# Kernel tuning notes

Hardware: AMD Instinct MI355X
Metric: run time of the kernel (lower is better)

The kernel has to match this reference:

```python
import jax, jax.numpy as jnp
import numpy as np

N_PAPER, N_AUTHOR = 200000, 100000
D_PAPER, D_AUTHOR = 128, 64
H, OUT = 64, 32
E_CITES, E_WRITES = 4000000, 2000000


def _gcn(x, W, b, src, dst, n):
    # GCNConv with default add_self_loops=True, symmetric normalization
    xl = x @ W
    deg = jnp.zeros((n,), xl.dtype).at[dst].add(1.0) + 1.0  # +1 for self loop
    dis = jax.lax.rsqrt(deg)
    norm = dis[src] * dis[dst]
    out = jax.ops.segment_sum(xl[src] * norm[:, None], dst, num_segments=n)
    out = out + xl * (dis * dis)[:, None]  # self-loop term: norm_ii = 1/deg_i
    return out + b


def _sage(x_src, x_dst, Wl, bl, Wr, src, dst, n_dst):
    # SAGEConv: mean neighbor aggregation -> lin_l, plus root lin_r on dst
    ones = jnp.ones(src.shape, x_src.dtype)
    cnt = jnp.maximum(jax.ops.segment_sum(ones, dst, num_segments=n_dst), 1.0)
    mean = jax.ops.segment_sum(x_src[src], dst, num_segments=n_dst) / cnt[:, None]
    return mean @ Wl + bl + x_dst @ Wr


def _gat(x_src, x_dst, Ws, Wd, a_s, a_d, b, src, dst, n_dst):
    # GATConv heads=1, bipartite, add_self_loops=False, leaky_relu slope 0.2
    xs = x_src @ Ws  # [Ns, H]
    xd = x_dst @ Wd  # [Nd, H]
    a_src = xs @ a_s  # [Ns]
    a_dst = xd @ a_d  # [Nd]
    e = a_src[src] + a_dst[dst]
    e = jnp.where(e > 0, e, 0.2 * e)
    m = jax.ops.segment_max(e, dst, num_segments=n_dst)
    m = jnp.where(jnp.isfinite(m), m, 0.0)  # nodes with no in-edges
    ex = jnp.exp(e - m[dst])
    denom = jax.ops.segment_sum(ex, dst, num_segments=n_dst)
    alpha = ex / denom[dst]
    out = jax.ops.segment_sum(alpha[:, None] * xs[src], dst, num_segments=n_dst)
    return out + b


def _forward(x_paper, x_author, params, cites_src, cites_dst, writes_src, writes_dst):
    for (gW, gb, sWl, sbl, sWr, aWs, aWd, aas, aad, ab) in params:
        p_gcn = _gcn(x_paper, gW, gb, cites_src, cites_dst, N_PAPER)
        p_sage = _sage(x_author, x_paper, sWl, sbl, sWr, writes_src, writes_dst, N_PAPER)
        # rev_writes: paper -> author, i.e. src=writes_dst (paper), dst=writes_src (author)
        a_gat = _gat(x_paper, x_author, aWs, aWd, aas, aad, ab, writes_dst, writes_src, N_AUTHOR)
        x_paper = jax.nn.relu(p_gcn + p_sage)  # HeteroConv aggr='sum'
        x_author = jax.nn.relu(a_gat)
    return x_paper, x_author


def setup_inputs() -> dict:
    key = jax.random.key(0)
    ks = jax.random.split(key, 40)
    rn = lambda i, shp, s=0.1: jax.random.normal(ks[i], shp, jnp.float32) * s
    inp = {}
    inp['x_paper'] = rn(0, (N_PAPER, D_PAPER), 1.0)
    inp['x_author'] = rn(1, (N_AUTHOR, D_AUTHOR), 1.0)
    dims = [(D_PAPER, D_AUTHOR), (H, H)]
    i = 2
    for l, (dp, da) in enumerate(dims):
        inp[f'gcn_W{l}'] = rn(i, (dp, H)); i += 1
        inp[f'gcn_b{l}'] = jnp.zeros((H,), jnp.float32)
        inp[f'sage_Wl{l}'] = rn(i, (da, H)); i += 1
        inp[f'sage_bl{l}'] = jnp.zeros((H,), jnp.float32)
        inp[f'sage_Wr{l}'] = rn(i, (dp, H)); i += 1
        inp[f'gat_Ws{l}'] = rn(i, (dp, H)); i += 1
        inp[f'gat_Wd{l}'] = rn(i, (da, H)); i += 1
        inp[f'gat_as{l}'] = rn(i, (H,)); i += 1
        inp[f'gat_ad{l}'] = rn(i, (H,)); i += 1
        inp[f'gat_b{l}'] = jnp.zeros((H,), jnp.float32)
    inp['lin_W'] = rn(i, (H, OUT)); i += 1
    inp['lin_b'] = jnp.zeros((OUT,), jnp.float32)
    inp['cites_src'] = jax.random.randint(ks[30], (E_CITES,), 0, N_PAPER)
    inp['cites_dst'] = jax.random.randint(ks[31], (E_CITES,), 0, N_PAPER)
    inp['writes_src'] = jax.random.randint(ks[32], (E_WRITES,), 0, N_AUTHOR)
    inp['writes_dst'] = jax.random.randint(ks[33], (E_WRITES,), 0, N_PAPER)
    return inp


def reference(x_paper, x_author,
              gcn_W0, gcn_b0, sage_Wl0, sage_bl0, sage_Wr0,
              gat_Ws0, gat_Wd0, gat_as0, gat_ad0, gat_b0,
              gcn_W1, gcn_b1, sage_Wl1, sage_bl1, sage_Wr1,
              gat_Ws1, gat_Wd1, gat_as1, gat_ad1, gat_b1,
              lin_W, lin_b,
              cites_src, cites_dst, writes_src, writes_dst):
    params = [
        (gcn_W0, gcn_b0, sage_Wl0, sage_bl0, sage_Wr0, gat_Ws0, gat_Wd0, gat_as0, gat_ad0, gat_b0),
        (gcn_W1, gcn_b1, sage_Wl1, sage_bl1, sage_Wr1, gat_Ws1, gat_Wd1, gat_as1, gat_ad1, gat_b1),
    ]
    _, x_author_out = _forward(x_paper, x_author, params, cites_src, cites_dst, writes_src, writes_dst)
    return x_author_out @ lin_W + lin_b
```

## Files before the change

kernel.cpp:

```cpp
#include <hip/hip_runtime.h>
#include <hip/hip_bf16.h>

#define NP 200000
#define NA 100000
#define DP 128
#define HD 64
#define EC 4000000
#define EW 2000000
#define NSCAN (2 * NP + NA)
#define NBUCK 8
#define CAPC 64
#define CAPW 48
#define CAPA 64

typedef __hip_bfloat16 bf16;
typedef __attribute__((ext_vector_type(8))) short short8;
typedef __attribute__((ext_vector_type(4))) float f32x4;

__device__ __forceinline__ float bf2f(bf16 h) { return __bfloat162float(h); }

__device__ __forceinline__ short8 pack8(float4 a, float4 b) {
    union {
        short8 s;
        unsigned u[4];
    } r;
    __hip_bfloat162 h;
    h = __float22bfloat162_rn(float2{a.x, a.y});
    r.u[0] = *reinterpret_cast<unsigned*>(&h);
    h = __float22bfloat162_rn(float2{a.z, a.w});
    r.u[1] = *reinterpret_cast<unsigned*>(&h);
    h = __float22bfloat162_rn(float2{b.x, b.y});
    r.u[2] = *reinterpret_cast<unsigned*>(&h);
    h = __float22bfloat162_rn(float2{b.z, b.w});
    r.u[3] = *reinterpret_cast<unsigned*>(&h);
    return r.s;
}


__global__ __launch_bounds__(256) void fill_pass_kernel(const int* __restrict__ cs,
                                                        const int* __restrict__ cd,
                                                        const int* __restrict__ ws,
                                                        const int* __restrict__ wd,
                                                        int* __restrict__ CUR,
                                                        int* __restrict__ colC,
                                                        int* __restrict__ colWd,
                                                        int* __restrict__ colWa, int bucket) {
    long i = (long)blockIdx.x * 256 + threadIdx.x;
    if (i < EC) {
        int d = __builtin_nontemporal_load(&cd[i]);
        if ((int)(((long)d * NBUCK) / NP) != bucket) return;
        int s = __builtin_nontemporal_load(&cs[i]);
        int pos = atomicAdd(&CUR[d * 4], 1);
        if (pos < CAPC) colC[(size_t)d * CAPC + pos] = s;
    } else if (i < (long)EC + EW) {
        long e = i - EC;
        int d = __builtin_nontemporal_load(&wd[e]);
        if ((int)(((long)d * NBUCK) / NP) != bucket) return;
        int s = __builtin_nontemporal_load(&ws[e]);
        int pos = atomicAdd(&CUR[(NP + d) * 4], 1);
        if (pos < CAPW) colWd[(size_t)d * CAPW + pos] = s;
    } else if (i < (long)EC + 2L * EW) {
        long e = i - EC - EW;
        int a = __builtin_nontemporal_load(&ws[e]);
        if ((int)(((long)a * NBUCK) / NA) != bucket) return;
        int d = __builtin_nontemporal_load(&wd[e]);
        int pos = atomicAdd(&CUR[(2 * NP + a) * 4], 1);
        if (pos < CAPA) colWa[(size_t)a * CAPA + pos] = d;
    }
}

__global__ __launch_bounds__(256) void finalize_kernel(const int* __restrict__ CUR,
                                                       float* __restrict__ dis,
                                                       float* __restrict__ invc) {
    int i = blockIdx.x * 256 + threadIdx.x;
    if (i >= NP) return;
    dis[i] = rsqrtf((float)CUR[i * 4] + 1.0f);
    invc[i] = 1.0f / fmaxf((float)CUR[(NP + i) * 4], 1.0f);
}


__global__ __launch_bounds__(256) void conv_author_kernel(const float* __restrict__ XA,
                                                          const float* __restrict__ wvec,
                                                          bf16* __restrict__ XAbf,
                                                          float* __restrict__ adst) {
    __shared__ float vs[64];
    if (threadIdx.x < 64) vs[threadIdx.x] = wvec[threadIdx.x];
    __syncthreads();
    int r = blockIdx.x * 4 + (threadIdx.x >> 6);
    int lane = threadIdx.x & 63;
    float x = XA[(size_t)r * 64 + lane];
    XAbf[(size_t)r * 64 + lane] = __float2bfloat16(x);
    float p = x * vs[lane];
#pragma unroll
    for (int o = 32; o > 0; o >>= 1) p += __shfl_xor(p, o, 64);
    if (lane == 0) adst[r] = p;
}


__global__ void wprep_kernel(const float* __restrict__ Wg, const float* __restrict__ Wl,
                             const float* __restrict__ Wr, const float* __restrict__ Ws0,
                             const float* __restrict__ Ws1, short* __restrict__ WF) {
    int bid = blockIdx.x;
    int lane = threadIdx.x;
    int q = lane & 15, g = lane >> 4;
    int m, r;
    size_t dst;
    if (bid < 16) {
        m = 0; r = bid; dst = 0;
    } else if (bid < 40) {
        m = 1; r = bid - 16; dst = 8192;
    } else if (bid < 56) {
        m = 2; r = bid - 40; dst = 20480;
    } else {
        m = 3; r = bid - 56; dst = 28672;
    }
    int ks = r >> 2, n = r & 3;
    int col = n * 16 + q;
    float v[8];
#pragma unroll
    for (int j = 0; j < 8; j++) {
        int kr = ks * 32 + g * 8 + j;
        float x;
        if (m == 0) x = Wg[(size_t)kr * 64 + col];
        else if (m == 1) x = (kr < 64) ? Wl[(size_t)kr * 64 + col] : Wr[(size_t)(kr - 64) * 64 + col];
        else if (m == 2) x = Ws0[(size_t)kr * 64 + col];
        else x = Ws1[(size_t)kr * 64 + col];
        v[j] = x;
    }
    short8 s = pack8(float4{v[0], v[1], v[2], v[3]}, float4{v[4], v[5], v[6], v[7]});
    *reinterpret_cast<short8*>(WF + dst + ((size_t)r * 64 + lane) * 8) = s;
}


template <int K, bool ABF16, bool ADOT>
__global__ __launch_bounds__(256) void mfma_gemm_kernel(const void* __restrict__ Xv,
                                                        const short* __restrict__ Wf,
                                                        bf16* __restrict__ outb,
                                                        const float* __restrict__ avec,
                                                        float* __restrict__ adot) {
    int tid = threadIdx.x;
    int lane = tid & 63, q = lane & 15, g = lane >> 4;
    int rw = blockIdx.x * 64 + (tid >> 6) * 16;
    int arow = rw + q;
    f32x4 acc[4];
#pragma unroll
    for (int n = 0; n < 4; n++) acc[n] = f32x4{0.f, 0.f, 0.f, 0.f};
#pragma unroll
    for (int ks = 0; ks < K / 32; ks++) {
        short8 af;
        if constexpr (ABF16) {
            af = *reinterpret_cast<const short8*>((const bf16*)Xv + (size_t)arow * K + ks * 32 +
                                                  g * 8);
        } else {
            const float* xr = (const float*)Xv + (size_t)arow * K + ks * 32 + g * 8;
            float4 a0 = *reinterpret_cast<const float4*>(xr);
            float4 a1 = *reinterpret_cast<const float4*>(xr + 4);
            af = pack8(a0, a1);
        }
#pragma unroll
        for (int n = 0; n < 4; n++) {
            short8 bfr = *reinterpret_cast<const short8*>(Wf + ((size_t)(ks * 4 + n) * 64 + lane) * 8);
            acc[n] = __builtin_amdgcn_mfma_f32_16x16x32_bf16(af, bfr, acc[n], 0, 0, 0);
        }
    }
    float av[4];
    if constexpr (ADOT) {
#pragma unroll
        for (int n = 0; n < 4; n++) av[n] = avec[n * 16 + q];
    }
#pragma unroll
    for (int j = 0; j < 4; j++) {
        int R = rw + g * 4 + j;
#pragma unroll
        for (int n = 0; n < 4; n++) {
            outb[(size_t)R * 64 + n * 16 + q] = __float2bfloat16(acc[n][j]);
        }
        if constexpr (ADOT) {
            float t = acc[0][j] * av[0] + acc[1][j] * av[1] + acc[2][j] * av[2] + acc[3][j] * av[3];
            t += __shfl_xor(t, 1, 64);
            t += __shfl_xor(t, 2, 64);
            t += __shfl_xor(t, 4, 64);
            t += __shfl_xor(t, 8, 64);
            if (q == 0) adot[R] = t;
        }
    }
}


__global__ __launch_bounds__(256) void mfma_sage_kernel(const bf16* B3bf,
                                                        const float* __restrict__ XP,
                                                        const float* __restrict__ B2,
                                                        const float* __restrict__ bl,
                                                        const short* __restrict__ Wf, bf16* P1) {
    int tid = threadIdx.x;
    int lane = tid & 63, q = lane & 15, g = lane >> 4;
    int rw = blockIdx.x * 64 + (tid >> 6) * 16;
    int arow = rw + q;
    f32x4 acc[4];
#pragma unroll
    for (int n = 0; n < 4; n++) acc[n] = f32x4{0.f, 0.f, 0.f, 0.f};
#pragma unroll
    for (int ks = 0; ks < 6; ks++) {
        short8 af;
        if (ks < 2) {
            af = *reinterpret_cast<const short8*>(B3bf + (size_t)arow * 64 + ks * 32 + g * 8);
        } else {
            const float* xr = XP + (size_t)arow * DP + (ks - 2) * 32 + g * 8;
            float4 a0 = *reinterpret_cast<const float4*>(xr);
            float4 a1 = *reinterpret_cast<const float4*>(xr + 4);
            af = pack8(a0, a1);
        }
#pragma unroll
        for (int n = 0; n < 4; n++) {
            short8 bfr = *reinterpret_cast<const short8*>(Wf + ((size_t)(ks * 4 + n) * 64 + lane) * 8);
            acc[n] = __builtin_amdgcn_mfma_f32_16x16x32_bf16(af, bfr, acc[n], 0, 0, 0);
        }
    }
    float blv[4];
#pragma unroll
    for (int n = 0; n < 4; n++) blv[n] = bl[n * 16 + q];
#pragma unroll
    for (int j = 0; j < 4; j++) {
        int R = rw + g * 4 + j;
#pragma unroll
        for (int n = 0; n < 4; n++) {
            int col = n * 16 + q;
            float v = acc[n][j] + B2[(size_t)R * 64 + col] + blv[n];
            P1[(size_t)R * 64 + col] = __float2bfloat16(fmaxf(v, 0.f));
        }
    }
}


__global__ __launch_bounds__(256) void gcn_gather_kernel(const bf16* __restrict__ B1,
                                                         const int* __restrict__ CUR,
                                                         const int* __restrict__ colC,
                                                         const float* __restrict__ dis,
                                                         const float* __restrict__ gb,
                                                         float* __restrict__ B2) {
    int node = __builtin_amdgcn_readfirstlane(blockIdx.x * 4 + (threadIdx.x >> 6));
    int lane = threadIdx.x & 63;
    int deg = min(CUR[node * 4], CAPC);
    const int* col = colC + (size_t)node * CAPC;
    float dd = dis[node];
    float self = bf2f(B1[(size_t)node * 64 + lane]);
    float acc = 0.f;
    int e = 0;
    for (; e + 8 <= deg; e += 8) {
        int s[8];
#pragma unroll
        for (int j = 0; j < 8; j++) s[j] = col[e + j];
        float n[8], v[8];
#pragma unroll
        for (int j = 0; j < 8; j++) n[j] = dis[s[j]];
#pragma unroll
        for (int j = 0; j < 8; j++) v[j] = bf2f(B1[(size_t)s[j] * 64 + lane]);
#pragma unroll
        for (int j = 0; j < 8; j++) acc += n[j] * v[j];
    }
    for (; e + 4 <= deg; e += 4) {
        int s0 = col[e], s1 = col[e + 1], s2 = col[e + 2], s3 = col[e + 3];
        float n0 = dis[s0], n1 = dis[s1], n2 = dis[s2], n3 = dis[s3];
        float v0 = bf2f(B1[(size_t)s0 * 64 + lane]);
        float v1 = bf2f(B1[(size_t)s1 * 64 + lane]);
        float v2 = bf2f(B1[(size_t)s2 * 64 + lane]);
        float v3 = bf2f(B1[(size_t)s3 * 64 + lane]);
        acc += n0 * v0 + n1 * v1;
        acc += n2 * v2 + n3 * v3;
    }
    for (; e < deg; e++) {
        int s = col[e];
        acc += dis[s] * bf2f(B1[(size_t)s * 64 + lane]);
    }
    B2[(size_t)node * 64 + lane] = acc * dd + self * dd * dd + gb[lane];
}


__global__ __launch_bounds__(256) void sage_gather_kernel(const bf16* __restrict__ XA,
                                                          const int* __restrict__ CUR,
                                                          const int* __restrict__ colWd,
                                                          const float* __restrict__ invc,
                                                          bf16* __restrict__ B3bf) {
    int node = __builtin_amdgcn_readfirstlane(blockIdx.x * 4 + (threadIdx.x >> 6));
    int lane = threadIdx.x & 63;
    int deg = min(CUR[(NP + node) * 4], CAPW);
    const int* col = colWd + (size_t)node * CAPW;
    float acc = 0.f;
    int e = 0;
    for (; e + 8 <= deg; e += 8) {
        int s[8];
#pragma unroll
        for (int j = 0; j < 8; j++) s[j] = col[e + j];
        float v[8];
#pragma unroll
        for (int j = 0; j < 8; j++) v[j] = bf2f(XA[(size_t)s[j] * 64 + lane]);
#pragma unroll
        for (int j = 0; j < 8; j++) acc += v[j];
    }
    for (; e < deg; e++) acc += bf2f(XA[(size_t)col[e] * 64 + lane]);
    B3bf[(size_t)node * 64 + lane] = __float2bfloat16(acc * invc[node]);
}


__global__ void matvec64_kernel(const float* __restrict__ Wd, const float* __restrict__ ad,
                                float* __restrict__ wvec) {
    int k = threadIdx.x;
    if (k >= 64) return;
    float s = 0.f;
    for (int c = 0; c < 64; c++) s += Wd[k * 64 + c] * ad[c];
    wvec[k] = s;
}

__device__ __forceinline__ float lrelu(float v) { return v > 0.f ? v : 0.2f * v; }


__global__ __launch_bounds__(256) void gat_l0_kernel(const bf16* __restrict__ XS,
                                                     const int* __restrict__ CUR,
                                                     const int* __restrict__ colA,
                                                     const float* __restrict__ asrc,
                                                     float* __restrict__ adst,
                                                     const float* __restrict__ ab,
                                                     const float* __restrict__ wvec1,
                                                     float* __restrict__ outA) {
    int a = __builtin_amdgcn_readfirstlane(blockIdx.x * 4 + (threadIdx.x >> 6));
    int lane = threadIdx.x & 63;
    int deg = min(CUR[(2 * NP + a) * 4], CAPA);
    const int* col = colA + (size_t)a * CAPA;
    float ada = adst[a];
    float acc = 0.f, den = 0.f;
    int e = 0;
    for (; e + 8 <= deg; e += 8) {
        int p[8];
#pragma unroll
        for (int j = 0; j < 8; j++) p[j] = col[e + j];
        float x[8], v[8];
#pragma unroll
        for (int j = 0; j < 8; j++) x[j] = __expf(lrelu(asrc[p[j]] + ada));
#pragma unroll
        for (int j = 0; j < 8; j++) v[j] = bf2f(XS[(size_t)p[j] * 64 + lane]);
#pragma unroll
        for (int j = 0; j < 8; j++) {
            den += x[j];
            acc += x[j] * v[j];
        }
    }
    for (; e < deg; e++) {
        int p = col[e];
        float x = __expf(lrelu(asrc[p] + ada));
        den += x;
        acc += x * bf2f(XS[(size_t)p * 64 + lane]);
    }
    float inv = den > 0.f ? 1.f / den : 0.f;
    float val = fmaxf(acc * inv + ab[lane], 0.f);
    outA[(size_t)a * 64 + lane] = val;
    float pr = val * wvec1[lane];
#pragma unroll
    for (int o = 32; o > 0; o >>= 1) pr += __shfl_xor(pr, o, 64);
    if (lane == 0) adst[a] = pr;
}


__global__ __launch_bounds__(256) void gat_final_kernel(const bf16* __restrict__ XS,
                                                        const int* __restrict__ CUR,
                                                        const int* __restrict__ colA,
                                                        const float* __restrict__ asrc,
                                                        const float* __restrict__ adst,
                                                        const float* __restrict__ ab,
                                                        const float* __restrict__ linW,
                                                        const float* __restrict__ linb,
                                                        float* __restrict__ out) {
    __shared__ float Ws[64 * 32];
    __shared__ float vbuf[4][64];
    __shared__ float lbs[32];
    int tid = threadIdx.x;
    for (int i = tid; i < 64 * 32; i += 256) Ws[i] = linW[i];
    if (tid < 32) lbs[tid] = linb[tid];
    __syncthreads();
    int wid = tid >> 6;
    int a = __builtin_amdgcn_readfirstlane(blockIdx.x * 4 + wid);
    int lane = tid & 63;
    int deg = min(CUR[(2 * NP + a) * 4], CAPA);
    const int* col = colA + (size_t)a * CAPA;
    float ada = adst[a];
    float acc = 0.f, den = 0.f;
    int e = 0;
    for (; e + 8 <= deg; e += 8) {
        int p[8];
#pragma unroll
        for (int j = 0; j < 8; j++) p[j] = col[e + j];
        float x[8], v[8];
#pragma unroll
        for (int j = 0; j < 8; j++) x[j] = __expf(lrelu(asrc[p[j]] + ada));
#pragma unroll
        for (int j = 0; j < 8; j++) v[j] = bf2f(XS[(size_t)p[j] * 64 + lane]);
#pragma unroll
        for (int j = 0; j < 8; j++) {
            den += x[j];
            acc += x[j] * v[j];
        }
    }
    for (; e < deg; e++) {
        int p = col[e];
        float x = __expf(lrelu(asrc[p] + ada));
        den += x;
        acc += x * bf2f(XS[(size_t)p * 64 + lane]);
    }
    float inv = den > 0.f ? 1.f / den : 0.f;
    vbuf[wid][lane] = fmaxf(acc * inv + ab[lane], 0.f);
    __syncthreads();
    if (tid < 128) {
        int w = tid >> 5, c = tid & 31;
        int node = blockIdx.x * 4 + w;
        float s = lbs[c];
#pragma unroll
        for (int k = 0; k < 64; k++) s += vbuf[w][k] * Ws[k * 32 + c];
        out[(size_t)node * 32 + c] = s;
    }
}


static inline int cdivi(long a, long b) { return (int)((a + b - 1) / b); }

extern "C" void kernel_launch(void* const* d_in, const int* in_sizes, int n_in, void* d_out,
                              int out_size, void* d_ws, size_t ws_size, hipStream_t stream) {
    const float* x_paper = (const float*)d_in[0];
    const float* x_author = (const float*)d_in[1];
    const float* gcn_W0 = (const float*)d_in[2];
    const float* gcn_b0 = (const float*)d_in[3];
    const float* sage_Wl0 = (const float*)d_in[4];
    const float* sage_bl0 = (const float*)d_in[5];
    const float* sage_Wr0 = (const float*)d_in[6];
    const float* gat_Ws0 = (const float*)d_in[7];
    const float* gat_Wd0 = (const float*)d_in[8];
    const float* gat_as0 = (const float*)d_in[9];
    const float* gat_ad0 = (const float*)d_in[10];
    const float* gat_b0 = (const float*)d_in[11];
    const float* gat_Ws1 = (const float*)d_in[17];
    const float* gat_Wd1 = (const float*)d_in[18];
    const float* gat_as1 = (const float*)d_in[19];
    const float* gat_ad1 = (const float*)d_in[20];
    const float* gat_b1 = (const float*)d_in[21];
    const float* lin_W = (const float*)d_in[22];
    const float* lin_b = (const float*)d_in[23];
    const int* cites_src = (const int*)d_in[24];
    const int* cites_dst = (const int*)d_in[25];
    const int* writes_src = (const int*)d_in[26];
    const int* writes_dst = (const int*)d_in[27];

    float* out = (float*)d_out;

    char* base = (char*)d_ws;
    bf16* BF = (bf16*)base;
    base += (size_t)NP * 64 * 2;
    float* B2 = (float*)base;
    base += (size_t)NP * 64 * 4;
    int* colC = (int*)base;
    bf16* B3bf = (bf16*)base;
    base += (size_t)NP * CAPC * 4;
    int* colWd = (int*)base;
    float* B5 = (float*)base;
    base += (size_t)NP * CAPW * 4;
    int* colWa = (int*)base;
    base += (size_t)NA * CAPA * 4;
    bf16* XAbf = (bf16*)base;
    base += (size_t)NA * 64 * 2;
    int* CUR = (int*)base;
    base += (size_t)NSCAN * 4 * 4;
    float* dis_p = (float*)base;
    float* invc = dis_p + NP;
    float* asrc = invc + NP;
    float* adst = asrc + NP;
    float* wvec0 = adst + NA;
    float* wvec1 = wvec0 + 64;
    short* WF = (short*)(wvec1 + 64);

    dim3 blk(256);
    const long ETOT = (long)EC + 2L * EW;

    hipMemsetAsync(CUR, 0, (size_t)NSCAN * 4 * 4, stream);
    matvec64_kernel<<<1, 64, 0, stream>>>(gat_Wd0, gat_ad0, wvec0);
    matvec64_kernel<<<1, 64, 0, stream>>>(gat_Wd1, gat_ad1, wvec1);
    wprep_kernel<<<64, 64, 0, stream>>>(gcn_W0, sage_Wl0, sage_Wr0, gat_Ws0, gat_Ws1, WF);

    for (int b = 0; b < NBUCK; b++) {
        fill_pass_kernel<<<cdivi(ETOT, 256), blk, 0, stream>>>(cites_src, cites_dst, writes_src,
                                                               writes_dst, CUR, colC, colWd,
                                                               colWa, b);
    }
    finalize_kernel<<<cdivi(NP, 256), blk, 0, stream>>>(CUR, dis_p, invc);

    conv_author_kernel<<<NA / 4, blk, 0, stream>>>(x_author, wvec0, XAbf, adst);

    mfma_gemm_kernel<DP, false, false><<<NP / 64, blk, 0, stream>>>(x_paper, WF, BF, nullptr,
                                                                    nullptr);
    gcn_gather_kernel<<<NP / 4, blk, 0, stream>>>(BF, CUR, colC, dis_p, gcn_b0, B2);

    sage_gather_kernel<<<NP / 4, blk, 0, stream>>>(XAbf, CUR, colWd, invc, B3bf);
    mfma_sage_kernel<<<NP / 64, blk, 0, stream>>>(B3bf, x_paper, B2, sage_bl0, WF + 8192, B3bf);

    mfma_gemm_kernel<DP, false, true><<<NP / 64, blk, 0, stream>>>(x_paper, WF + 20480, BF,
                                                                   gat_as0, asrc);
    gat_l0_kernel<<<NA / 4, blk, 0, stream>>>(BF, CUR, colWa, asrc, adst, gat_b0, wvec1, B5);

    mfma_gemm_kernel<HD, true, true><<<NP / 64, blk, 0, stream>>>(B3bf, WF + 28672, BF, gat_as1,
                                                                  asrc);
    gat_final_kernel<<<NA / 4, blk, 0, stream>>>(BF, CUR, colWa, asrc, adst, gat_b1, lin_W, lin_b,
                                                 out);
}
```

Baseline: 944.4 us.

## Overlap CSR fill passes with GCN GEMM and author conversion; half-wave gathers

Each of the eight bucketed fill passes now also runs a slice of the first GCN GEMM and of the author bf16 conversion inside one hybrid kernel, so latency-bound atomic scatter work overlaps with compute. The writes-edge pass reads each edge once and fills both the paper-side and author-side adjacency lists, which cuts index reads. The gather kernels now split the 64 lanes into two halves that each handle alternate neighbours with bf16 pair loads, then combine the halves with a cross-lane shuffle. The risks are branch divergence inside the hybrid kernel, higher register pressure from launch_bounds(256,8), and a changed floating-point summation order.

```diff
diff --git a/kernel.cpp b/kernel.cpp
--- a/kernel.cpp
+++ b/kernel.cpp
@@ -13,11 +13,26 @@
 #define CAPW 48
 #define CAPA 64
 
+#define FILLB ((EC + EW + 255) / 256)
+#define NRB (NP / 64)
+#define GB ((NRB + NBUCK - 1) / NBUCK)
+#define CONVB (NA / 4 / NBUCK)
+
 typedef __hip_bfloat16 bf16;
 typedef __attribute__((ext_vector_type(8))) short short8;
 typedef __attribute__((ext_vector_type(4))) float f32x4;
 
 __device__ __forceinline__ float bf2f(bf16 h) { return __bfloat162float(h); }
+
+__device__ __forceinline__ float2 bfpair(const bf16* p) {
+    __hip_bfloat162 h = *reinterpret_cast<const __hip_bfloat162*>(p);
+    return __bfloat1622float2(h);
+}
+
+__device__ __forceinline__ void bfstore2(bf16* p, float x, float y) {
+    __hip_bfloat162 h = __float22bfloat162_rn(float2{x, y});
+    *reinterpret_cast<unsigned*>(p) = *reinterpret_cast<unsigned*>(&h);
+}
 
 __device__ __forceinline__ short8 pack8(float4 a, float4 b) {
     union {
@@ -37,35 +52,102 @@
 }
 
 
-__global__ __launch_bounds__(256) void fill_pass_kernel(const int* __restrict__ cs,
-                                                        const int* __restrict__ cd,
-                                                        const int* __restrict__ ws,
-                                                        const int* __restrict__ wd,
-                                                        int* __restrict__ CUR,
-                                                        int* __restrict__ colC,
-                                                        int* __restrict__ colWd,
-                                                        int* __restrict__ colWa, int bucket) {
-    long i = (long)blockIdx.x * 256 + threadIdx.x;
-    if (i < EC) {
-        int d = __builtin_nontemporal_load(&cd[i]);
-        if ((int)(((long)d * NBUCK) / NP) != bucket) return;
-        int s = __builtin_nontemporal_load(&cs[i]);
-        int pos = atomicAdd(&CUR[d * 4], 1);
-        if (pos < CAPC) colC[(size_t)d * CAPC + pos] = s;
-    } else if (i < (long)EC + EW) {
-        long e = i - EC;
-        int d = __builtin_nontemporal_load(&wd[e]);
-        if ((int)(((long)d * NBUCK) / NP) != bucket) return;
-        int s = __builtin_nontemporal_load(&ws[e]);
-        int pos = atomicAdd(&CUR[(NP + d) * 4], 1);
-        if (pos < CAPW) colWd[(size_t)d * CAPW + pos] = s;
-    } else if (i < (long)EC + 2L * EW) {
-        long e = i - EC - EW;
-        int a = __builtin_nontemporal_load(&ws[e]);
-        if ((int)(((long)a * NBUCK) / NA) != bucket) return;
-        int d = __builtin_nontemporal_load(&wd[e]);
-        int pos = atomicAdd(&CUR[(2 * NP + a) * 4], 1);
-        if (pos < CAPA) colWa[(size_t)a * CAPA + pos] = d;
+template <int K, bool ABF16, bool ADOT>
+__device__ __forceinline__ void mfma_body(const void* __restrict__ Xv,
+                                          const short* __restrict__ Wf, bf16* __restrict__ outb,
+                                          const float* __restrict__ avec,
+                                          float* __restrict__ adot, int rowblock, int tid) {
+    int lane = tid & 63, q = lane & 15, g = lane >> 4;
+    int rw = rowblock * 64 + (tid >> 6) * 16;
+    int arow = rw + q;
+    f32x4 acc[4];
+#pragma unroll
+    for (int n = 0; n < 4; n++) acc[n] = f32x4{0.f, 0.f, 0.f, 0.f};
+#pragma unroll
+    for (int ks = 0; ks < K / 32; ks++) {
+        short8 af;
+        if constexpr (ABF16) {
+            af = *reinterpret_cast<const short8*>((const bf16*)Xv + (size_t)arow * K + ks * 32 +
+                                                  g * 8);
+        } else {
+            const float* xr = (const float*)Xv + (size_t)arow * K + ks * 32 + g * 8;
+            float4 a0 = *reinterpret_cast<const float4*>(xr);
+            float4 a1 = *reinterpret_cast<const float4*>(xr + 4);
+            af = pack8(a0, a1);
+        }
+#pragma unroll
+        for (int n = 0; n < 4; n++) {
+            short8 bfr =
+                *reinterpret_cast<const short8*>(Wf + ((size_t)(ks * 4 + n) * 64 + lane) * 8);
+            acc[n] = __builtin_amdgcn_mfma_f32_16x16x32_bf16(af, bfr, acc[n], 0, 0, 0);
+        }
+    }
+    float av[4];
+    if constexpr (ADOT) {
+#pragma unroll
+        for (int n = 0; n < 4; n++) av[n] = avec[n * 16 + q];
+    }
+#pragma unroll
+    for (int j = 0; j < 4; j++) {
+        int R = rw + g * 4 + j;
+#pragma unroll
+        for (int n = 0; n < 4; n++) {
+            outb[(size_t)R * 64 + n * 16 + q] = __float2bfloat16(acc[n][j]);
+        }
+        if constexpr (ADOT) {
+            float t = acc[0][j] * av[0] + acc[1][j] * av[1] + acc[2][j] * av[2] + acc[3][j] * av[3];
+            t += __shfl_xor(t, 1, 64);
+            t += __shfl_xor(t, 2, 64);
+            t += __shfl_xor(t, 4, 64);
+            t += __shfl_xor(t, 8, 64);
+            if (q == 0) adot[R] = t;
+        }
+    }
+}
+
+
+__global__ __launch_bounds__(256, 8) void hybrid_kernel(
+    const int* __restrict__ cs, const int* __restrict__ cd, const int* __restrict__ ws,
+    const int* __restrict__ wd, int* __restrict__ CUR, int* __restrict__ colC,
+    int* __restrict__ colWd, int* __restrict__ colWa, int bucket, const float* __restrict__ XP,
+    const short* __restrict__ WFg, bf16* __restrict__ BF, const float* __restrict__ XA,
+    const float* __restrict__ wvec0, bf16* __restrict__ XAbf, float* __restrict__ adst) {
+    int bid = blockIdx.x;
+    int tid = threadIdx.x;
+    if (bid < FILLB) {
+        long i = (long)bid * 256 + tid;
+        if (i < EC) {
+            int d = __builtin_nontemporal_load(&cd[i]);
+            if ((int)(((long)d * NBUCK) / NP) != bucket) return;
+            int s = __builtin_nontemporal_load(&cs[i]);
+            int pos = atomicAdd(&CUR[d * 4], 1);
+            if (pos < CAPC) colC[(size_t)d * CAPC + pos] = s;
+        } else if (i < (long)EC + EW) {
+            long e = i - EC;
+            int d = __builtin_nontemporal_load(&wd[e]);
+            int a = __builtin_nontemporal_load(&ws[e]);
+            if ((int)(((long)d * NBUCK) / NP) == bucket) {
+                int pos = atomicAdd(&CUR[(NP + d) * 4], 1);
+                if (pos < CAPW) colWd[(size_t)d * CAPW + pos] = a;
+            }
+            if ((int)(((long)a * NBUCK) / NA) == bucket) {
+                int pos = atomicAdd(&CUR[(2 * NP + a) * 4], 1);
+                if (pos < CAPA) colWa[(size_t)a * CAPA + pos] = d;
+            }
+        }
+    } else if (bid < FILLB + GB) {
+        int rb = bucket * GB + (bid - FILLB);
+        if (rb >= NRB) return;
+        mfma_body<DP, false, false>(XP, WFg, BF, nullptr, nullptr, rb, tid);
+    } else {
+        int a = (bucket * CONVB + (bid - FILLB - GB)) * 4 + (tid >> 6);
+        int lane = tid & 63;
+        float x = XA[(size_t)a * 64 + lane];
+        XAbf[(size_t)a * 64 + lane] = __float2bfloat16(x);
+        float p = x * wvec0[lane];
+#pragma unroll
+        for (int o = 32; o > 0; o >>= 1) p += __shfl_xor(p, o, 64);
+        if (lane == 0) adst[a] = p;
     }
 }
 
@@ -76,24 +158,6 @@
     if (i >= NP) return;
     dis[i] = rsqrtf((float)CUR[i * 4] + 1.0f);
     invc[i] = 1.0f / fmaxf((float)CUR[(NP + i) * 4], 1.0f);
-}
-
-
-__global__ __launch_bounds__(256) void conv_author_kernel(const float* __restrict__ XA,
-                                                          const float* __restrict__ wvec,
-                                                          bf16* __restrict__ XAbf,
-                                                          float* __restrict__ adst) {
-    __shared__ float vs[64];
-    if (threadIdx.x < 64) vs[threadIdx.x] = wvec[threadIdx.x];
-    __syncthreads();
-    int r = blockIdx.x * 4 + (threadIdx.x >> 6);
-    int lane = threadIdx.x & 63;
-    float x = XA[(size_t)r * 64 + lane];
-    XAbf[(size_t)r * 64 + lane] = __float2bfloat16(x);
-    float p = x * vs[lane];
-#pragma unroll
-    for (int o = 32; o > 0; o >>= 1) p += __shfl_xor(p, o, 64);
-    if (lane == 0) adst[r] = p;
 }
 
 
@@ -138,52 +202,7 @@
                                                         bf16* __restrict__ outb,
                                                         const float* __restrict__ avec,
                                                         float* __restrict__ adot) {
-    int tid = threadIdx.x;
-    int lane = tid & 63, q = lane & 15, g = lane >> 4;
-    int rw = blockIdx.x * 64 + (tid >> 6) * 16;
-    int arow = rw + q;
-    f32x4 acc[4];
-#pragma unroll
-    for (int n = 0; n < 4; n++) acc[n] = f32x4{0.f, 0.f, 0.f, 0.f};
-#pragma unroll
-    for (int ks = 0; ks < K / 32; ks++) {
-        short8 af;
-        if constexpr (ABF16) {
-            af = *reinterpret_cast<const short8*>((const bf16*)Xv + (size_t)arow * K + ks * 32 +
-                                                  g * 8);
-        } else {
-            const float* xr = (const float*)Xv + (size_t)arow * K + ks * 32 + g * 8;
-            float4 a0 = *reinterpret_cast<const float4*>(xr);
-            float4 a1 = *reinterpret_cast<const float4*>(xr + 4);
-            af = pack8(a0, a1);
-        }
-#pragma unroll
-        for (int n = 0; n < 4; n++) {
-            short8 bfr = *reinterpret_cast<const short8*>(Wf + ((size_t)(ks * 4 + n) * 64 + lane) * 8);
-            acc[n] = __builtin_amdgcn_mfma_f32_16x16x32_bf16(af, bfr, acc[n], 0, 0, 0);
-        }
-    }
-    float av[4];
-    if constexpr (ADOT) {
-#pragma unroll
-        for (int n = 0; n < 4; n++) av[n] = avec[n * 16 + q];
-    }
-#pragma unroll
-    for (int j = 0; j < 4; j++) {
-        int R = rw + g * 4 + j;
-#pragma unroll
-        for (int n = 0; n < 4; n++) {
-            outb[(size_t)R * 64 + n * 16 + q] = __float2bfloat16(acc[n][j]);
-        }
-        if constexpr (ADOT) {
-            float t = acc[0][j] * av[0] + acc[1][j] * av[1] + acc[2][j] * av[2] + acc[3][j] * av[3];
-            t += __shfl_xor(t, 1, 64);
-            t += __shfl_xor(t, 2, 64);
-            t += __shfl_xor(t, 4, 64);
-            t += __shfl_xor(t, 8, 64);
-            if (q == 0) adot[R] = t;
-        }
-    }
+    mfma_body<K, ABF16, ADOT>(Xv, Wf, outb, avec, adot, blockIdx.x, threadIdx.x);
 }
 
 
@@ -212,7 +231,8 @@
         }
 #pragma unroll
         for (int n = 0; n < 4; n++) {
-            short8 bfr = *reinterpret_cast<const short8*>(Wf + ((size_t)(ks * 4 + n) * 64 + lane) * 8);
+            short8 bfr =
+                *reinterpret_cast<const short8*>(Wf + ((size_t)(ks * 4 + n) * 64 + lane) * 8);
             acc[n] = __builtin_amdgcn_mfma_f32_16x16x32_bf16(af, bfr, acc[n], 0, 0, 0);
         }
     }
@@ -240,39 +260,46 @@
                                                          float* __restrict__ B2) {
     int node = __builtin_amdgcn_readfirstlane(blockIdx.x * 4 + (threadIdx.x >> 6));
     int lane = threadIdx.x & 63;
+    int half = lane >> 5, c = lane & 31;
     int deg = min(CUR[node * 4], CAPC);
     const int* col = colC + (size_t)node * CAPC;
     float dd = dis[node];
-    float self = bf2f(B1[(size_t)node * 64 + lane]);
-    float acc = 0.f;
+    float2 acc = {0.f, 0.f};
     int e = 0;
-    for (; e + 8 <= deg; e += 8) {
+    for (; e + 16 <= deg; e += 16) {
         int s[8];
 #pragma unroll
-        for (int j = 0; j < 8; j++) s[j] = col[e + j];
-        float n[8], v[8];
+        for (int j = 0; j < 8; j++) s[j] = col[e + 2 * j + half];
+        float n[8];
 #pragma unroll
         for (int j = 0; j < 8; j++) n[j] = dis[s[j]];
-#pragma unroll
-        for (int j = 0; j < 8; j++) v[j] = bf2f(B1[(size_t)s[j] * 64 + lane]);
-#pragma unroll
-        for (int j = 0; j < 8; j++) acc += n[j] * v[j];
-    }
-    for (; e + 4 <= deg; e += 4) {
-        int s0 = col[e], s1 = col[e + 1], s2 = col[e + 2], s3 = col[e + 3];
-        float n0 = dis[s0], n1 = dis[s1], n2 = dis[s2], n3 = dis[s3];
-        float v0 = bf2f(B1[(size_t)s0 * 64 + lane]);
-        float v1 = bf2f(B1[(size_t)s1 * 64 + lane]);
-        float v2 = bf2f(B1[(size_t)s2 * 64 + lane]);
-        float v3 = bf2f(B1[(size_t)s3 * 64 + lane]);
-        acc += n0 * v0 + n1 * v1;
-        acc += n2 * v2 + n3 * v3;
-    }
-    for (; e < deg; e++) {
-        int s = col[e];
-        acc += dis[s] * bf2f(B1[(size_t)s * 64 + lane]);
-    }
-    B2[(size_t)node * 64 + lane] = acc * dd + self * dd * dd + gb[lane];
+        float2 v[8];
+#pragma unroll
+        for (int j = 0; j < 8; j++) v[j] = bfpair(B1 + (size_t)s[j] * 64 + 2 * c);
+#pragma unroll
+        for (int j = 0; j < 8; j++) {
+            acc.x += n[j] * v[j].x;
+            acc.y += n[j] * v[j].y;
+        }
+    }
+    for (; e < deg; e += 2) {
+        int idx = e + half;
+        bool act = idx < deg;
+        int s = col[act ? idx : e];
+        float n = act ? dis[s] : 0.f;
+        float2 v = bfpair(B1 + (size_t)s * 64 + 2 * c);
+        acc.x += n * v.x;
+        acc.y += n * v.y;
+    }
+    acc.x += __shfl_xor(acc.x, 32, 64);
+    acc.y += __shfl_xor(acc.y, 32, 64);
+    if (half == 0) {
+        float2 self = bfpair(B1 + (size_t)node * 64 + 2 * c);
+        float2 o;
+        o.x = acc.x * dd + self.x * dd * dd + gb[2 * c];
+        o.y = acc.y * dd + self.y * dd * dd + gb[2 * c + 1];
+        *reinterpret_cast<float2*>(B2 + (size_t)node * 64 + 2 * c) = o;
+    }
 }
 
 
@@ -283,22 +310,39 @@
                                                           bf16* __restrict__ B3bf) {
     int node = __builtin_amdgcn_readfirstlane(blockIdx.x * 4 + (threadIdx.x >> 6));
     int lane = threadIdx.x & 63;
+    int half = lane >> 5, c = lane & 31;
     int deg = min(CUR[(NP + node) * 4], CAPW);
     const int* col = colWd + (size_t)node * CAPW;
-    float acc = 0.f;
+    float2 acc = {0.f, 0.f};
     int e = 0;
-    for (; e + 8 <= deg; e += 8) {
+    for (; e + 16 <= deg; e += 16) {
         int s[8];
 #pragma unroll
-        for (int j = 0; j < 8; j++) s[j] = col[e + j];
-        float v[8];
-#pragma unroll
-        for (int j = 0; j < 8; j++) v[j] = bf2f(XA[(size_t)s[j] * 64 + lane]);
-#pragma unroll
-        for (int j = 0; j < 8; j++) acc += v[j];
-    }
-    for (; e < deg; e++) acc += bf2f(XA[(size_t)col[e] * 64 + lane]);
-    B3bf[(size_t)node * 64 + lane] = __float2bfloat16(acc * invc[node]);
+        for (int j = 0; j < 8; j++) s[j] = col[e + 2 * j + half];
+        float2 v[8];
+#pragma unroll
+        for (int j = 0; j < 8; j++) v[j] = bfpair(XA + (size_t)s[j] * 64 + 2 * c);
+#pragma unroll
+        for (int j = 0; j < 8; j++) {
+            acc.x += v[j].x;
+            acc.y += v[j].y;
+        }
+    }
+    for (; e < deg; e += 2) {
+        int idx = e + half;
+        bool act = idx < deg;
+        int s = col[act ? idx : e];
+        float2 v = bfpair(XA + (size_t)s * 64 + 2 * c);
+        float n = act ? 1.f : 0.f;
+        acc.x += n * v.x;
+        acc.y += n * v.y;
+    }
+    acc.x += __shfl_xor(acc.x, 32, 64);
+    acc.y += __shfl_xor(acc.y, 32, 64);
+    if (half == 0) {
+        float ic = invc[node];
+        bfstore2(B3bf + (size_t)node * 64 + 2 * c, acc.x * ic, acc.y * ic);
+    }
 }
 
 
@@ -324,39 +368,56 @@
                                                      float* __restrict__ outA) {
     int a = __builtin_amdgcn_readfirstlane(blockIdx.x * 4 + (threadIdx.x >> 6));
     int lane = threadIdx.x & 63;
+    int half = lane >> 5, c = lane & 31;
     int deg = min(CUR[(2 * NP + a) * 4], CAPA);
     const int* col = colA + (size_t)a * CAPA;
     float ada = adst[a];
-    float acc = 0.f, den = 0.f;
+    float2 acc = {0.f, 0.f};
+    float den = 0.f;
     int e = 0;
-    for (; e + 8 <= deg; e += 8) {
-        int p[8];
-#pragma unroll
-        for (int j = 0; j < 8; j++) p[j] = col[e + j];
-        float x[8], v[8];
-#pragma unroll
-        for (int j = 0; j < 8; j++) x[j] = __expf(lrelu(asrc[p[j]] + ada));
-#pragma unroll
-        for (int j = 0; j < 8; j++) v[j] = bf2f(XS[(size_t)p[j] * 64 + lane]);
+    for (; e + 16 <= deg; e += 16) {
+        int s[8];
+#pragma unroll
+        for (int j = 0; j < 8; j++) s[j] = col[e + 2 * j + half];
+        float x[8];
+#pragma unroll
+        for (int j = 0; j < 8; j++) x[j] = __expf(lrelu(asrc[s[j]] + ada));
+        float2 v[8];
+#pragma unroll
+        for (int j = 0; j < 8; j++) v[j] = bfpair(XS + (size_t)s[j] * 64 + 2 * c);
 #pragma unroll
         for (int j = 0; j < 8; j++) {
             den += x[j];
-            acc += x[j] * v[j];
-        }
-    }
-    for (; e < deg; e++) {
-        int p = col[e];
-        float x = __expf(lrelu(asrc[p] + ada));
+            acc.x += x[j] * v[j].x;
+            acc.y += x[j] * v[j].y;
+        }
+    }
+    for (; e < deg; e += 2) {
+        int idx = e + half;
+        bool act = idx < deg;
+        int s = col[act ? idx : e];
+        float x = act ? __expf(lrelu(asrc[s] + ada)) : 0.f;
+        float2 v = bfpair(XS + (size_t)s * 64 + 2 * c);
         den += x;
-        acc += x * bf2f(XS[(size_t)p * 64 + lane]);
-    }
+        acc.x += x * v.x;
+        acc.y += x * v.y;
+    }
+    acc.x += __shfl_xor(acc.x, 32, 64);
+    acc.y += __shfl_xor(acc.y, 32, 64);
+    den += __shfl_xor(den, 32, 64);
     float inv = den > 0.f ? 1.f / den : 0.f;
-    float val = fmaxf(acc * inv + ab[lane], 0.f);
-    outA[(size_t)a * 64 + lane] = val;
-    float pr = val * wvec1[lane];
-#pragma unroll
-    for (int o = 32; o > 0; o >>= 1) pr += __shfl_xor(pr, o, 64);
-    if (lane == 0) adst[a] = pr;
+    float vx = fmaxf(acc.x * inv + ab[2 * c], 0.f);
+    float vy = fmaxf(acc.y * inv + ab[2 * c + 1], 0.f);
+    float pr = vx * wvec1[2 * c] + vy * wvec1[2 * c + 1];
+    pr += __shfl_xor(pr, 1, 64);
+    pr += __shfl_xor(pr, 2, 64);
+    pr += __shfl_xor(pr, 4, 64);
+    pr += __shfl_xor(pr, 8, 64);
+    pr += __shfl_xor(pr, 16, 64);
+    if (half == 0) {
+        *reinterpret_cast<float2*>(outA + (size_t)a * 64 + 2 * c) = float2{vx, vy};
+        if (c == 0) adst[a] = pr;
+    }
 }
 
 
@@ -379,42 +440,56 @@
     int wid = tid >> 6;
     int a = __builtin_amdgcn_readfirstlane(blockIdx.x * 4 + wid);
     int lane = tid & 63;
+    int half = lane >> 5, c = lane & 31;
     int deg = min(CUR[(2 * NP + a) * 4], CAPA);
     const int* col = colA + (size_t)a * CAPA;
     float ada = adst[a];
-    float acc = 0.f, den = 0.f;
+    float2 acc = {0.f, 0.f};
+    float den = 0.f;
     int e = 0;
-    for (; e + 8 <= deg; e += 8) {
-        int p[8];
-#pragma unroll
-        for (int j = 0; j < 8; j++) p[j] = col[e + j];
-        float x[8], v[8];
-#pragma unroll
-        for (int j = 0; j < 8; j++) x[j] = __expf(lrelu(asrc[p[j]] + ada));
-#pragma unroll
-        for (int j = 0; j < 8; j++) v[j] = bf2f(XS[(size_t)p[j] * 64 + lane]);
+    for (; e + 16 <= deg; e += 16) {
+        int s[8];
+#pragma unroll
+        for (int j = 0; j < 8; j++) s[j] = col[e + 2 * j + half];
+        float x[8];
+#pragma unroll
+        for (int j = 0; j < 8; j++) x[j] = __expf(lrelu(asrc[s[j]] + ada));
+        float2 v[8];
+#pragma unroll
+        for (int j = 0; j < 8; j++) v[j] = bfpair(XS + (size_t)s[j] * 64 + 2 * c);
 #pragma unroll
         for (int j = 0; j < 8; j++) {
             den += x[j];
-            acc += x[j] * v[j];
-        }
-    }
-    for (; e < deg; e++) {
-        int p = col[e];
-        float x = __expf(lrelu(asrc[p] + ada));
+            acc.x += x[j] * v[j].x;
+            acc.y += x[j] * v[j].y;
+        }
+    }
+    for (; e < deg; e += 2) {
+        int idx = e + half;
+        bool act = idx < deg;
+        int s = col[act ? idx : e];
+        float x = act ? __expf(lrelu(asrc[s] + ada)) : 0.f;
+        float2 v = bfpair(XS + (size_t)s * 64 + 2 * c);
         den += x;
-        acc += x * bf2f(XS[(size_t)p * 64 + lane]);
-    }
+        acc.x += x * v.x;
+        acc.y += x * v.y;
+    }
+    acc.x += __shfl_xor(acc.x, 32, 64);
+    acc.y += __shfl_xor(acc.y, 32, 64);
+    den += __shfl_xor(den, 32, 64);
     float inv = den > 0.f ? 1.f / den : 0.f;
-    vbuf[wid][lane] = fmaxf(acc * inv + ab[lane], 0.f);
+    if (half == 0) {
+        vbuf[wid][2 * c] = fmaxf(acc.x * inv + ab[2 * c], 0.f);
+        vbuf[wid][2 * c + 1] = fmaxf(acc.y * inv + ab[2 * c + 1], 0.f);
+    }
     __syncthreads();
     if (tid < 128) {
-        int w = tid >> 5, c = tid & 31;
+        int w = tid >> 5, cc = tid & 31;
         int node = blockIdx.x * 4 + w;
-        float s = lbs[c];
-#pragma unroll
-        for (int k = 0; k < 64; k++) s += vbuf[w][k] * Ws[k * 32 + c];
-        out[(size_t)node * 32 + c] = s;
+        float s = lbs[cc];
+#pragma unroll
+        for (int k = 0; k < 64; k++) s += vbuf[w][k] * Ws[k * 32 + cc];
+        out[(size_t)node * 32 + cc] = s;
     }
 }
 
@@ -475,7 +550,6 @@
     short* WF = (short*)(wvec1 + 64);
 
     dim3 blk(256);
-    const long ETOT = (long)EC + 2L * EW;
 
     hipMemsetAsync(CUR, 0, (size_t)NSCAN * 4 * 4, stream);
     matvec64_kernel<<<1, 64, 0, stream>>>(gat_Wd0, gat_ad0, wvec0);
@@ -483,27 +557,23 @@
     wprep_kernel<<<64, 64, 0, stream>>>(gcn_W0, sage_Wl0, sage_Wr0, gat_Ws0, gat_Ws1, WF);
 
     for (int b = 0; b < NBUCK; b++) {
-        fill_pass_kernel<<<cdivi(ETOT, 256), blk, 0, stream>>>(cites_src, cites_dst, writes_src,
-                                                               writes_dst, CUR, colC, colWd,
-                                                               colWa, b);
+        hybrid_kernel<<<FILLB + GB + CONVB, blk, 0, stream>>>(
+            cites_src, cites_dst, writes_src, writes_dst, CUR, colC, colWd, colWa, b, x_paper, WF,
+            BF, x_author, wvec0, XAbf, adst);
     }
     finalize_kernel<<<cdivi(NP, 256), blk, 0, stream>>>(CUR, dis_p, invc);
 
-    conv_author_kernel<<<NA / 4, blk, 0, stream>>>(x_author, wvec0, XAbf, adst);
-
-    mfma_gemm_kernel<DP, false, false><<<NP / 64, blk, 0, stream>>>(x_paper, WF, BF, nullptr,
-                                                                    nullptr);
     gcn_gather_kernel<<<NP / 4, blk, 0, stream>>>(BF, CUR, colC, dis_p, gcn_b0, B2);
 
     sage_gather_kernel<<<NP / 4, blk, 0, stream>>>(XAbf, CUR, colWd, invc, B3bf);
     mfma_sage_kernel<<<NP / 64, blk, 0, stream>>>(B3bf, x_paper, B2, sage_bl0, WF + 8192, B3bf);
 
-    mfma_gemm_kernel<DP, false, true><<<NP / 64, blk, 0, stream>>>(x_paper, WF + 20480, BF,
-                                                                   gat_as0, asrc);
+    mfma_gemm_kernel<DP, false, true><<<NRB, blk, 0, stream>>>(x_paper, WF + 20480, BF, gat_as0,
+                                                               asrc);
     gat_l0_kernel<<<NA / 4, blk, 0, stream>>>(BF, CUR, colWa, asrc, adst, gat_b0, wvec1, B5);
 
-    mfma_gemm_kernel<HD, true, true><<<NP / 64, blk, 0, stream>>>(B3bf, WF + 28672, BF, gat_as1,
-                                                                  asrc);
+    mfma_gemm_kernel<HD, true, true><<<NRB, blk, 0, stream>>>(B3bf, WF + 28672, BF, gat_as1,
+                                                              asrc);
     gat_final_kernel<<<NA / 4, blk, 0, stream>>>(BF, CUR, colWa, asrc, adst, gat_b1, lin_W, lin_b,
                                                  out);
 }
```

Result: slower. 1.003 ms (+6.2%).

## Prescale GCN features by source norm, merge writes fill passes, drop dead store

Applied to the files above, without the earlier changes.

Three changes. The GCN GEMM epilogue now multiplies each output row by dis[row], so the gather no longer loads dis per neighbour and the self-loop term folds into the accumulator. The two writes-edge fill passes are merged into one thread per edge that reads src and dst once and inserts into both adjacency lists, which shrinks the launch grid of each of the eight bucket passes. The unused author-feature store in gat_l0 is removed. The trade-off is that the prescaled values are rounded to bf16 after scaling, which slightly changes numerics.

```diff
diff --git a/kernel.cpp b/kernel.cpp
--- a/kernel.cpp
+++ b/kernel.cpp
@@ -55,17 +55,15 @@
     } else if (i < (long)EC + EW) {
         long e = i - EC;
         int d = __builtin_nontemporal_load(&wd[e]);
-        if ((int)(((long)d * NBUCK) / NP) != bucket) return;
-        int s = __builtin_nontemporal_load(&ws[e]);
-        int pos = atomicAdd(&CUR[(NP + d) * 4], 1);
-        if (pos < CAPW) colWd[(size_t)d * CAPW + pos] = s;
-    } else if (i < (long)EC + 2L * EW) {
-        long e = i - EC - EW;
         int a = __builtin_nontemporal_load(&ws[e]);
-        if ((int)(((long)a * NBUCK) / NA) != bucket) return;
-        int d = __builtin_nontemporal_load(&wd[e]);
-        int pos = atomicAdd(&CUR[(2 * NP + a) * 4], 1);
-        if (pos < CAPA) colWa[(size_t)a * CAPA + pos] = d;
+        if ((int)(((long)d * NBUCK) / NP) == bucket) {
+            int pos = atomicAdd(&CUR[(NP + d) * 4], 1);
+            if (pos < CAPW) colWd[(size_t)d * CAPW + pos] = a;
+        }
+        if ((int)(((long)a * NBUCK) / NA) == bucket) {
+            int pos = atomicAdd(&CUR[(2 * NP + a) * 4], 1);
+            if (pos < CAPA) colWa[(size_t)a * CAPA + pos] = d;
+        }
     }
 }
 
@@ -132,12 +130,13 @@
 }
 
 
-template <int K, bool ABF16, bool ADOT>
+template <int K, bool ABF16, bool ADOT, bool SCALE>
 __global__ __launch_bounds__(256) void mfma_gemm_kernel(const void* __restrict__ Xv,
                                                         const short* __restrict__ Wf,
                                                         bf16* __restrict__ outb,
                                                         const float* __restrict__ avec,
-                                                        float* __restrict__ adot) {
+                                                        float* __restrict__ adot,
+                                                        const float* __restrict__ rowscale) {
     int tid = threadIdx.x;
     int lane = tid & 63, q = lane & 15, g = lane >> 4;
     int rw = blockIdx.x * 64 + (tid >> 6) * 16;
@@ -159,7 +158,8 @@
         }
 #pragma unroll
         for (int n = 0; n < 4; n++) {
-            short8 bfr = *reinterpret_cast<const short8*>(Wf + ((size_t)(ks * 4 + n) * 64 + lane) * 8);
+            short8 bfr =
+                *reinterpret_cast<const short8*>(Wf + ((size_t)(ks * 4 + n) * 64 + lane) * 8);
             acc[n] = __builtin_amdgcn_mfma_f32_16x16x32_bf16(af, bfr, acc[n], 0, 0, 0);
         }
     }
@@ -171,9 +171,11 @@
 #pragma unroll
     for (int j = 0; j < 4; j++) {
         int R = rw + g * 4 + j;
+        float sc = 1.f;
+        if constexpr (SCALE) sc = rowscale[R];
 #pragma unroll
         for (int n = 0; n < 4; n++) {
-            outb[(size_t)R * 64 + n * 16 + q] = __float2bfloat16(acc[n][j]);
+            outb[(size_t)R * 64 + n * 16 + q] = __float2bfloat16(acc[n][j] * sc);
         }
         if constexpr (ADOT) {
             float t = acc[0][j] * av[0] + acc[1][j] * av[1] + acc[2][j] * av[2] + acc[3][j] * av[3];
@@ -212,7 +214,8 @@
         }
 #pragma unroll
         for (int n = 0; n < 4; n++) {
-            short8 bfr = *reinterpret_cast<const short8*>(Wf + ((size_t)(ks * 4 + n) * 64 + lane) * 8);
+            short8 bfr =
+                *reinterpret_cast<const short8*>(Wf + ((size_t)(ks * 4 + n) * 64 + lane) * 8);
             acc[n] = __builtin_amdgcn_mfma_f32_16x16x32_bf16(af, bfr, acc[n], 0, 0, 0);
         }
     }
@@ -243,36 +246,29 @@
     int deg = min(CUR[node * 4], CAPC);
     const int* col = colC + (size_t)node * CAPC;
     float dd = dis[node];
-    float self = bf2f(B1[(size_t)node * 64 + lane]);
-    float acc = 0.f;
+    float acc = bf2f(B1[(size_t)node * 64 + lane]);
     int e = 0;
     for (; e + 8 <= deg; e += 8) {
         int s[8];
 #pragma unroll
         for (int j = 0; j < 8; j++) s[j] = col[e + j];
-        float n[8], v[8];
-#pragma unroll
-        for (int j = 0; j < 8; j++) n[j] = dis[s[j]];
+        float v[8];
 #pragma unroll
         for (int j = 0; j < 8; j++) v[j] = bf2f(B1[(size_t)s[j] * 64 + lane]);
 #pragma unroll
-        for (int j = 0; j < 8; j++) acc += n[j] * v[j];
+        for (int j = 0; j < 8; j++) acc += v[j];
     }
     for (; e + 4 <= deg; e += 4) {
         int s0 = col[e], s1 = col[e + 1], s2 = col[e + 2], s3 = col[e + 3];
-        float n0 = dis[s0], n1 = dis[s1], n2 = dis[s2], n3 = dis[s3];
         float v0 = bf2f(B1[(size_t)s0 * 64 + lane]);
         float v1 = bf2f(B1[(size_t)s1 * 64 + lane]);
         float v2 = bf2f(B1[(size_t)s2 * 64 + lane]);
         float v3 = bf2f(B1[(size_t)s3 * 64 + lane]);
-        acc += n0 * v0 + n1 * v1;
-        acc += n2 * v2 + n3 * v3;
-    }
-    for (; e < deg; e++) {
-        int s = col[e];
-        acc += dis[s] * bf2f(B1[(size_t)s * 64 + lane]);
-    }
-    B2[(size_t)node * 64 + lane] = acc * dd + self * dd * dd + gb[lane];
+        acc += v0 + v1;
+        acc += v2 + v3;
+    }
+    for (; e < deg; e++) acc += bf2f(B1[(size_t)col[e] * 64 + lane]);
+    B2[(size_t)node * 64 + lane] = acc * dd + gb[lane];
 }
 
 
@@ -320,8 +316,7 @@
                                                      const float* __restrict__ asrc,
                                                      float* __restrict__ adst,
                                                      const float* __restrict__ ab,
-                                                     const float* __restrict__ wvec1,
-                                                     float* __restrict__ outA) {
+                                                     const float* __restrict__ wvec1) {
     int a = __builtin_amdgcn_readfirstlane(blockIdx.x * 4 + (threadIdx.x >> 6));
     int lane = threadIdx.x & 63;
     int deg = min(CUR[(2 * NP + a) * 4], CAPA);
@@ -352,7 +347,6 @@
     }
     float inv = den > 0.f ? 1.f / den : 0.f;
     float val = fmaxf(acc * inv + ab[lane], 0.f);
-    outA[(size_t)a * 64 + lane] = val;
     float pr = val * wvec1[lane];
 #pragma unroll
     for (int o = 32; o > 0; o >>= 1) pr += __shfl_xor(pr, o, 64);
@@ -458,7 +452,6 @@
     bf16* B3bf = (bf16*)base;
     base += (size_t)NP * CAPC * 4;
     int* colWd = (int*)base;
-    float* B5 = (float*)base;
     base += (size_t)NP * CAPW * 4;
     int* colWa = (int*)base;
     base += (size_t)NA * CAPA * 4;
@@ -475,7 +468,7 @@
     short* WF = (short*)(wvec1 + 64);
 
     dim3 blk(256);
-    const long ETOT = (long)EC + 2L * EW;
+    const long EMERGED = (long)EC + EW;
 
     hipMemsetAsync(CUR, 0, (size_t)NSCAN * 4 * 4, stream);
     matvec64_kernel<<<1, 64, 0, stream>>>(gat_Wd0, gat_ad0, wvec0);
@@ -483,27 +476,28 @@
     wprep_kernel<<<64, 64, 0, stream>>>(gcn_W0, sage_Wl0, sage_Wr0, gat_Ws0, gat_Ws1, WF);
 
     for (int b = 0; b < NBUCK; b++) {
-        fill_pass_kernel<<<cdivi(ETOT, 256), blk, 0, stream>>>(cites_src, cites_dst, writes_src,
-                                                               writes_dst, CUR, colC, colWd,
-                                                               colWa, b);
+        fill_pass_kernel<<<cdivi(EMERGED, 256), blk, 0, stream>>>(cites_src, cites_dst,
+                                                                  writes_src, writes_dst, CUR,
+                                                                  colC, colWd, colWa, b);
     }
     finalize_kernel<<<cdivi(NP, 256), blk, 0, stream>>>(CUR, dis_p, invc);
 
     conv_author_kernel<<<NA / 4, blk, 0, stream>>>(x_author, wvec0, XAbf, adst);
 
-    mfma_gemm_kernel<DP, false, false><<<NP / 64, blk, 0, stream>>>(x_paper, WF, BF, nullptr,
-                                                                    nullptr);
+    mfma_gemm_kernel<DP, false, false, true><<<NP / 64, blk, 0, stream>>>(x_paper, WF, BF,
+                                                                          nullptr, nullptr,
+                                                                          dis_p);
     gcn_gather_kernel<<<NP / 4, blk, 0, stream>>>(BF, CUR, colC, dis_p, gcn_b0, B2);
 
     sage_gather_kernel<<<NP / 4, blk, 0, stream>>>(XAbf, CUR, colWd, invc, B3bf);
     mfma_sage_kernel<<<NP / 64, blk, 0, stream>>>(B3bf, x_paper, B2, sage_bl0, WF + 8192, B3bf);
 
-    mfma_gemm_kernel<DP, false, true><<<NP / 64, blk, 0, stream>>>(x_paper, WF + 20480, BF,
-                                                                   gat_as0, asrc);
-    gat_l0_kernel<<<NA / 4, blk, 0, stream>>>(BF, CUR, colWa, asrc, adst, gat_b0, wvec1, B5);
-
-    mfma_gemm_kernel<HD, true, true><<<NP / 64, blk, 0, stream>>>(B3bf, WF + 28672, BF, gat_as1,
-                                                                  asrc);
+    mfma_gemm_kernel<DP, false, true, false><<<NP / 64, blk, 0, stream>>>(x_paper, WF + 20480, BF,
+                                                                          gat_as0, asrc, nullptr);
+    gat_l0_kernel<<<NA / 4, blk, 0, stream>>>(BF, CUR, colWa, asrc, adst, gat_b0, wvec1);
+
+    mfma_gemm_kernel<HD, true, true, false><<<NP / 64, blk, 0, stream>>>(B3bf, WF + 28672, BF,
+                                                                         gat_as1, asrc, nullptr);
     gat_final_kernel<<<NA / 4, blk, 0, stream>>>(BF, CUR, colWa, asrc, adst, gat_b1, lin_W, lin_b,
                                                  out);
 }
```

New measurement: 892.8 us. 5.5% less time.
